# Optimization experiments

Hardware: AMD Instinct MI355X
Metric: run time of the kernel (lower is better)

The kernel has to match this reference:

```python
import jax, jax.numpy as jnp
import numpy as np

N, E, IN_F, H1, F1, H2, F2, OUT_F = 50000, 800000, 128, 4, 32, 1, 64, 2
NEG_SLOPE = 0.2  # PyG GATConv default


def setup_inputs() -> dict:
    key = jax.random.key(0)
    ks = jax.random.split(key, 10)
    p = lambda k, shp: jax.random.normal(k, shp, jnp.float32) * 0.1
    return {
        "x": jax.random.normal(ks[0], (N, IN_F), jnp.float32),
        "edge_index": jax.random.randint(ks[1], (2, E), 0, N),
        "W1": p(ks[2], (IN_F, H1 * F1)),
        "att_s1": p(ks[3], (H1, F1)),
        "att_d1": p(ks[4], (H1, F1)),
        "b1": jnp.zeros((H1 * F1,), jnp.float32),
        "W2": p(ks[5], (H1 * F1, H2 * F2)),
        "att_s2": p(ks[6], (H2, F2)),
        "att_d2": p(ks[7], (H2, F2)),
        "b2": jnp.zeros((F2,), jnp.float32),
        "Wl": p(ks[8], (F2, OUT_F)),
        "bl": jnp.zeros((OUT_F,), jnp.float32),
    }


def _gat_conv(x, src, dst, W, att_s, att_d, bias, concat):
    # PyG GATConv: per-head linear, leaky-relu attention logits,
    # segment-softmax over incoming edges of each dst, scatter-add aggregate.
    n = x.shape[0]
    H, F = att_s.shape
    h = (x @ W).reshape(n, H, F)                        # [N, H, F]
    a_s = jnp.einsum('nhf,hf->nh', h, att_s)            # [N, H]
    a_d = jnp.einsum('nhf,hf->nh', h, att_d)
    logits = jax.nn.leaky_relu(a_s[src] + a_d[dst], NEG_SLOPE)  # [Etot, H]
    m = jax.ops.segment_max(logits, dst, num_segments=n)
    e = jnp.exp(logits - m[dst])
    denom = jax.ops.segment_sum(e, dst, num_segments=n)
    alpha = e / denom[dst]                              # segment softmax
    msg = h[src] * alpha[:, :, None]                    # [Etot, H, F]
    out = jax.ops.segment_sum(msg, dst, num_segments=n)  # [N, H, F]
    out = out.reshape(n, H * F) if concat else out.mean(axis=1)
    return out + bias


def reference(x, edge_index, W1, att_s1, att_d1, b1, W2, att_s2, att_d2, b2, Wl, bl):
    n = x.shape[0]
    loops = jnp.arange(n, dtype=edge_index.dtype)       # add_self_loops=True
    src = jnp.concatenate([edge_index[0], loops])
    dst = jnp.concatenate([edge_index[1], loops])
    h = jax.nn.elu(_gat_conv(x, src, dst, W1, att_s1, att_d1, b1, True))
    h = jax.nn.elu(_gat_conv(h, src, dst, W2, att_s2, att_d2, b2, False))
    pooled = h.sum(axis=0, keepdims=True)               # global_add_pool, batch=0
    out = pooled @ Wl + bl
    return pooled, out
```

## Files before the change

### kernel.cpp

```cpp
#include <hip/hip_runtime.h>

#define N_NODES 50000
#define N_EDGES 800000
#define NB 196
#define P1_BLOCKS 256
#define EPB 3125
#define BH_SIZE (NB * P1_BLOCKS)
#define GEMM_BLOCKS ((N_NODES + 63) / 64)

__device__ __forceinline__ float lrelu(float x) { return fmaxf(x, 0.2f * x); }
__device__ __forceinline__ float elu(float x) { return x > 0.f ? x : __expf(x) - 1.f; }

typedef float f32x2 __attribute__((ext_vector_type(2)));

__device__ __forceinline__ float bfl(unsigned u) { return __uint_as_float(u << 16); }
__device__ __forceinline__ float bfh(unsigned u) { return __uint_as_float(u & 0xffff0000u); }
__device__ __forceinline__ unsigned f2bf_rn(float x) {
  unsigned u = __float_as_uint(x);
  return (u + 0x7fffu + ((u >> 16) & 1u)) >> 16;
}
__device__ __forceinline__ unsigned pack2bf(float a, float b) {
  return f2bf_rn(a) | (f2bf_rn(b) << 16);
}

__device__ __forceinline__ int block_excl_scan(int v, int* total_out) {
  int lane = threadIdx.x & 63;
  int wid = threadIdx.x >> 6;
  int x = v;
#pragma unroll
  for (int off = 1; off < 64; off <<= 1) {
    int u = __shfl_up(x, off);
    if (lane >= off) x += u;
  }
  __shared__ int wsum[4];
  if (lane == 63) wsum[wid] = x;
  __syncthreads();
  int add = 0;
#pragma unroll
  for (int k = 0; k < 4; ++k)
    if (k < wid) add += wsum[k];
  if (total_out) *total_out = wsum[0] + wsum[1] + wsum[2] + wsum[3];
  return x + add - v;
}

__global__ __launch_bounds__(256) void hist1_kernel(const int* __restrict__ ei, int* __restrict__ bh) {
  __shared__ int cnt[NB];
  for (int t = threadIdx.x; t < NB; t += 256) cnt[t] = 0;
  __syncthreads();
  int start = blockIdx.x * EPB;
  for (int i = start + threadIdx.x; i < start + EPB; i += 256)
    atomicAdd(&cnt[ei[N_EDGES + i] >> 8], 1);
  __syncthreads();
  for (int t = threadIdx.x; t < NB; t += 256)
    bh[t * P1_BLOCKS + blockIdx.x] = cnt[t];
}

__global__ __launch_bounds__(256) void scan_part_kernel(const int* __restrict__ bh, int* __restrict__ bhP,
                                                        int* __restrict__ blocksum) {
  int g = blockIdx.x * 256 + threadIdx.x;
  int v = bh[g];
  int total;
  int ex = block_excl_scan(v, &total);
  bhP[g] = ex;
  if (threadIdx.x == 0) blocksum[blockIdx.x] = total;
}

__global__ __launch_bounds__(256) void scan_top_kernel(const int* __restrict__ blocksum, int* __restrict__ blockoff) {
  int t = threadIdx.x;
  int v = (t < NB) ? blocksum[t] : 0;
  int ex = block_excl_scan(v, nullptr);
  if (t < NB) blockoff[t] = ex;
}

__global__ __launch_bounds__(256) void scatter1_kernel(const int* __restrict__ ei, const int* __restrict__ bhP,
                                                       const int* __restrict__ blockoff, int2* __restrict__ eb) {
  __shared__ int cur[NB];
  for (int t = threadIdx.x; t < NB; t += 256) cur[t] = 0;
  __syncthreads();
  int start = blockIdx.x * EPB;
  for (int i = start + threadIdx.x; i < start + EPB; i += 256) {
    int dst = ei[N_EDGES + i];
    int src = ei[i];
    int bin = dst >> 8;
    int r = atomicAdd(&cur[bin], 1);
    int idx = bin * P1_BLOCKS + blockIdx.x;
    int pos = bhP[idx] + blockoff[bin] + r;
    eb[pos] = make_int2(src, dst);
  }
}

__global__ __launch_bounds__(256) void bucket_csr_kernel(const int2* __restrict__ eb, const int* __restrict__ blockoff,
                                                         int* __restrict__ rowptrF, int* __restrict__ col) {
  __shared__ int cnt[256];
  __shared__ int basel[256];
  __shared__ int cur[256];
  int b = blockIdx.x;
  int t = threadIdx.x;
  cnt[t] = 0;
  cur[t] = 0;
  __syncthreads();
  int start = blockoff[b];
  int end = (b == NB - 1) ? N_EDGES : blockoff[b + 1];
  for (int i = start + t; i < end; i += 256)
    atomicAdd(&cnt[eb[i].y & 255], 1);
  __syncthreads();
  int ex = block_excl_scan(cnt[t], nullptr);
  basel[t] = start + ex;
  int g = b * 256 + t;
  if (g < N_NODES) rowptrF[g] = start + ex;
  if (g == N_NODES) rowptrF[N_NODES] = N_EDGES;
  __syncthreads();
  for (int i = start + t; i < end; i += 256) {
    int2 e = eb[i];
    int d8 = e.y & 255;
    int r = atomicAdd(&cur[d8], 1);
    col[basel[d8] + r] = e.x;
  }
}

#define XS_STRIDE 36
template <int COLS, bool ABF16>
__device__ __forceinline__ void gemm_body(int bx, const void* __restrict__ Ap, const float* __restrict__ W,
                                          const float* __restrict__ atts, const float* __restrict__ attd,
                                          unsigned* __restrict__ Yb, float* __restrict__ as_out,
                                          float* __restrict__ ad_out) {
  constexpr int CPT = COLS / 16;
  constexpr int G = COLS / 4;
  __shared__ float ws[32 * COLS];
  __shared__ float xs[64 * XS_STRIDE];
  int t = threadIdx.x;
  int rbase = bx * 64;
  int tx = t & 15, ty = t >> 4;
  float acc[4][CPT];
#pragma unroll
  for (int r = 0; r < 4; ++r)
#pragma unroll
    for (int c = 0; c < CPT; ++c) acc[r][c] = 0.f;

  const float4* W4 = (const float4*)W;
  float4* ws4 = (float4*)ws;
  for (int kt = 0; kt < 4; ++kt) {
    for (int i = t; i < 32 * G; i += 256) {
      int k = i / G;
      int g = i - k * G;
      int c4g = g & (CPT / 4 - 1);
      int txg = g / (CPT / 4);
      ws4[k * G + c4g * 16 + txg] = W4[kt * 32 * G + i];
    }
    if constexpr (ABF16) {
      const uint4* A4 = (const uint4*)Ap;
      {
        int i = t;
        int row = i >> 2, q = i & 3;
        int gr = rbase + row; if (gr >= N_NODES) gr = N_NODES - 1;
        uint4 u = A4[gr * 16 + kt * 4 + q];
        float4 lo = make_float4(bfl(u.x), bfh(u.x), bfl(u.y), bfh(u.y));
        float4 hi = make_float4(bfl(u.z), bfh(u.z), bfl(u.w), bfh(u.w));
        float4* dst = (float4*)&xs[row * XS_STRIDE + q * 8];
        dst[0] = lo; dst[1] = hi;
      }
    } else {
      const float4* A4 = (const float4*)Ap;
      for (int i = t; i < 512; i += 256) {
        int row = i >> 3, kc = i & 7;
        int gr = rbase + row; if (gr >= N_NODES) gr = N_NODES - 1;
        *(float4*)&xs[row * XS_STRIDE + kc * 4] = A4[gr * 32 + kt * 8 + kc];
      }
    }
    __syncthreads();
#pragma unroll 8
    for (int k = 0; k < 32; ++k) {
      float xr[4];
#pragma unroll
      for (int r = 0; r < 4; ++r) xr[r] = xs[(ty * 4 + r) * XS_STRIDE + k];
#pragma unroll
      for (int c4 = 0; c4 < CPT / 4; ++c4) {
        float4 wv = ws4[k * G + c4 * 16 + tx];
#pragma unroll
        for (int r = 0; r < 4; ++r) {
          acc[r][c4 * 4 + 0] += xr[r] * wv.x;
          acc[r][c4 * 4 + 1] += xr[r] * wv.y;
          acc[r][c4 * 4 + 2] += xr[r] * wv.z;
          acc[r][c4 * 4 + 3] += xr[r] * wv.w;
        }
      }
    }
    __syncthreads();
  }

  if constexpr (COLS == 128) {
    int h = tx >> 2;
    int base = h * 32 + (tx & 3) * 8;
#pragma unroll
    for (int r = 0; r < 4; ++r) {
      float ps = 0.f, pd = 0.f;
#pragma unroll
      for (int c = 0; c < 8; ++c) {
        ps += acc[r][c] * atts[base + c];
        pd += acc[r][c] * attd[base + c];
      }
      ps += __shfl_xor(ps, 1); pd += __shfl_xor(pd, 1);
      ps += __shfl_xor(ps, 2); pd += __shfl_xor(pd, 2);
      int row = rbase + ty * 4 + r;
      if ((tx & 3) == 0 && row < N_NODES) {
        as_out[row * 4 + h] = ps;
        ad_out[row * 4 + h] = pd;
      }
    }
  } else {
#pragma unroll
    for (int r = 0; r < 4; ++r) {
      float ps = 0.f, pd = 0.f;
#pragma unroll
      for (int c = 0; c < 4; ++c) {
        ps += acc[r][c] * atts[tx * 4 + c];
        pd += acc[r][c] * attd[tx * 4 + c];
      }
#pragma unroll
      for (int off = 1; off < 16; off <<= 1) {
        ps += __shfl_xor(ps, off);
        pd += __shfl_xor(pd, off);
      }
      int row = rbase + ty * 4 + r;
      if (tx == 0 && row < N_NODES) {
        as_out[row] = ps;
        ad_out[row] = pd;
      }
    }
  }

#pragma unroll
  for (int r = 0; r < 4; ++r) {
    int row = rbase + ty * 4 + r;
    if (row < N_NODES) {
      if constexpr (CPT == 8) {
        unsigned lo = __builtin_amdgcn_cvt_pk_fp8_f32(acc[r][0], acc[r][1], 0, false);
        lo = __builtin_amdgcn_cvt_pk_fp8_f32(acc[r][2], acc[r][3], lo, true);
        unsigned hi = __builtin_amdgcn_cvt_pk_fp8_f32(acc[r][4], acc[r][5], 0, false);
        hi = __builtin_amdgcn_cvt_pk_fp8_f32(acc[r][6], acc[r][7], hi, true);
        ((uint2*)Yb)[row * 16 + tx] = make_uint2(lo, hi);
      } else {
        unsigned u = __builtin_amdgcn_cvt_pk_fp8_f32(acc[r][0], acc[r][1], 0, false);
        u = __builtin_amdgcn_cvt_pk_fp8_f32(acc[r][2], acc[r][3], u, true);
        Yb[row * 16 + tx] = u;
      }
    }
  }
}

__global__ __launch_bounds__(256) void gemm128_kernel(const float* __restrict__ x, const float* __restrict__ W1,
                                                      const float* __restrict__ atts, const float* __restrict__ attd,
                                                      unsigned* __restrict__ h1b, float* __restrict__ as1,
                                                      float* __restrict__ ad1) {
  gemm_body<128, false>(blockIdx.x, x, W1, atts, attd, h1b, as1, ad1);
}

__global__ __launch_bounds__(256) void gemm64_kernel(const unsigned* __restrict__ h1eb, const float* __restrict__ W2,
                                                     const float* __restrict__ atts, const float* __restrict__ attd,
                                                     unsigned* __restrict__ h2b, float* __restrict__ as2,
                                                     float* __restrict__ ad2) {
  gemm_body<64, true>(blockIdx.x, h1eb, W2, atts, attd, h2b, as2, ad2);
}

__global__ __launch_bounds__(256) void agg1_kernel(const uint2* __restrict__ h1f8, const int* __restrict__ rowptr,
                                                   const int* __restrict__ col, const float* __restrict__ as1,
                                                   const float* __restrict__ ad1, const float4* __restrict__ b1v,
                                                   uint4* __restrict__ h1eb4) {
  int n = (blockIdx.x * 256 + threadIdx.x) >> 6;
  int lane = threadIdx.x & 63;
  int slot = lane >> 4;
  int fo = lane & 15;
  int h = fo >> 2;
  int beg = rowptr[n], end = rowptr[n + 1];
  float adh = ad1[n * 4 + h];

  f32x2 acc2[4];
#pragma unroll
  for (int j = 0; j < 4; ++j) acc2[j] = (f32x2){0.f, 0.f};
  float esum = 0.f;

#define ACC_EDGE1(E)                                               \
  {                                                                \
    int src = col[E];                                              \
    float a = __expf(lrelu(as1[src * 4 + h] + adh));               \
    esum += a;                                                     \
    f32x2 av = {a, a};                                             \
    uint2 uu = h1f8[src * 16 + fo];                                \
    f32x2 p0 = __builtin_amdgcn_cvt_pk_f32_fp8(uu.x, false);       \
    f32x2 p1 = __builtin_amdgcn_cvt_pk_f32_fp8(uu.x, true);        \
    f32x2 p2 = __builtin_amdgcn_cvt_pk_f32_fp8(uu.y, false);       \
    f32x2 p3 = __builtin_amdgcn_cvt_pk_f32_fp8(uu.y, true);        \
    acc2[0] += av * p0; acc2[1] += av * p1;                        \
    acc2[2] += av * p2; acc2[3] += av * p3;                        \
  }

  int i = beg;
  for (; i + 16 <= end; i += 16) {
#pragma unroll
    for (int u = 0; u < 4; ++u) ACC_EDGE1(i + u * 4 + slot);
  }
  for (; i + 4 <= end; i += 4) ACC_EDGE1(i + slot);
  int rem = end - i;
  if (slot < rem) ACC_EDGE1(i + slot);
#undef ACC_EDGE1
  if (slot == 0) {
    float a = __expf(lrelu(as1[n * 4 + h] + adh));
    esum += a;
    f32x2 av = {a, a};
    uint2 uu = h1f8[n * 16 + fo];
    f32x2 p0 = __builtin_amdgcn_cvt_pk_f32_fp8(uu.x, false);
    f32x2 p1 = __builtin_amdgcn_cvt_pk_f32_fp8(uu.x, true);
    f32x2 p2 = __builtin_amdgcn_cvt_pk_f32_fp8(uu.y, false);
    f32x2 p3 = __builtin_amdgcn_cvt_pk_f32_fp8(uu.y, true);
    acc2[0] += av * p0; acc2[1] += av * p1;
    acc2[2] += av * p2; acc2[3] += av * p3;
  }
#pragma unroll
  for (int j = 0; j < 4; ++j) {
    acc2[j].x += __shfl_xor(acc2[j].x, 16);
    acc2[j].y += __shfl_xor(acc2[j].y, 16);
    acc2[j].x += __shfl_xor(acc2[j].x, 32);
    acc2[j].y += __shfl_xor(acc2[j].y, 32);
  }
  esum += __shfl_xor(esum, 16);
  esum += __shfl_xor(esum, 32);
  if (slot == 0) {
    float dsc = 1.f / esum;
    float4 b0 = b1v[fo * 2], b1 = b1v[fo * 2 + 1];
    float f0 = elu(acc2[0].x * dsc + b0.x), f1 = elu(acc2[0].y * dsc + b0.y);
    float f2 = elu(acc2[1].x * dsc + b0.z), f3 = elu(acc2[1].y * dsc + b0.w);
    float f4 = elu(acc2[2].x * dsc + b1.x), f5 = elu(acc2[2].y * dsc + b1.y);
    float f6 = elu(acc2[3].x * dsc + b1.z), f7 = elu(acc2[3].y * dsc + b1.w);
    uint4 o;
    o.x = pack2bf(f0, f1); o.y = pack2bf(f2, f3);
    o.z = pack2bf(f4, f5); o.w = pack2bf(f6, f7);
    h1eb4[n * 16 + fo] = o;
  }
}

__global__ __launch_bounds__(256) void agg2_kernel(const uint2* __restrict__ h2f8, const int* __restrict__ rowptr,
                                                   const int* __restrict__ col, const float* __restrict__ as2,
                                                   const float* __restrict__ ad2, const float4* __restrict__ b2v,
                                                   float* __restrict__ pooled) {
  __shared__ float red[4][64];
  int n = (blockIdx.x * 256 + threadIdx.x) >> 6;
  int lane = threadIdx.x & 63;
  int wid = threadIdx.x >> 6;
  int slot = lane >> 3;
  int fo = lane & 7;
  int beg = rowptr[n], end = rowptr[n + 1];
  float ad = ad2[n];

  f32x2 acc2[4];
#pragma unroll
  for (int j = 0; j < 4; ++j) acc2[j] = (f32x2){0.f, 0.f};
  float esum = 0.f;

#define ACC_EDGE2(E)                                               \
  {                                                                \
    int src = col[E];                                              \
    float a = __expf(lrelu(as2[src] + ad));                        \
    esum += a;                                                     \
    f32x2 av = {a, a};                                             \
    uint2 uu = h2f8[src * 8 + fo];                                 \
    f32x2 p0 = __builtin_amdgcn_cvt_pk_f32_fp8(uu.x, false);       \
    f32x2 p1 = __builtin_amdgcn_cvt_pk_f32_fp8(uu.x, true);        \
    f32x2 p2 = __builtin_amdgcn_cvt_pk_f32_fp8(uu.y, false);       \
    f32x2 p3 = __builtin_amdgcn_cvt_pk_f32_fp8(uu.y, true);        \
    acc2[0] += av * p0; acc2[1] += av * p1;                        \
    acc2[2] += av * p2; acc2[3] += av * p3;                        \
  }

  int i = beg;
  for (; i + 32 <= end; i += 32) {
#pragma unroll
    for (int u = 0; u < 4; ++u) ACC_EDGE2(i + u * 8 + slot);
  }
  for (; i + 8 <= end; i += 8) ACC_EDGE2(i + slot);
  int rem = end - i;
  if (slot < rem) ACC_EDGE2(i + slot);
#undef ACC_EDGE2
  if (slot == 0) {
    float a = __expf(lrelu(as2[n] + ad));
    esum += a;
    f32x2 av = {a, a};
    uint2 uu = h2f8[n * 8 + fo];
    f32x2 p0 = __builtin_amdgcn_cvt_pk_f32_fp8(uu.x, false);
    f32x2 p1 = __builtin_amdgcn_cvt_pk_f32_fp8(uu.x, true);
    f32x2 p2 = __builtin_amdgcn_cvt_pk_f32_fp8(uu.y, false);
    f32x2 p3 = __builtin_amdgcn_cvt_pk_f32_fp8(uu.y, true);
    acc2[0] += av * p0; acc2[1] += av * p1;
    acc2[2] += av * p2; acc2[3] += av * p3;
  }
#pragma unroll
  for (int j = 0; j < 4; ++j) {
#pragma unroll
    for (int off = 8; off <= 32; off <<= 1) {
      acc2[j].x += __shfl_xor(acc2[j].x, off);
      acc2[j].y += __shfl_xor(acc2[j].y, off);
    }
  }
  esum += __shfl_xor(esum, 8);
  esum += __shfl_xor(esum, 16);
  esum += __shfl_xor(esum, 32);
  if (slot == 0) {
    float dsc = 1.f / esum;
    float4 b0 = b2v[fo * 2], b1 = b2v[fo * 2 + 1];
    red[wid][fo * 8 + 0] = elu(acc2[0].x * dsc + b0.x);
    red[wid][fo * 8 + 1] = elu(acc2[0].y * dsc + b0.y);
    red[wid][fo * 8 + 2] = elu(acc2[1].x * dsc + b0.z);
    red[wid][fo * 8 + 3] = elu(acc2[1].y * dsc + b0.w);
    red[wid][fo * 8 + 4] = elu(acc2[2].x * dsc + b1.x);
    red[wid][fo * 8 + 5] = elu(acc2[2].y * dsc + b1.y);
    red[wid][fo * 8 + 6] = elu(acc2[3].x * dsc + b1.z);
    red[wid][fo * 8 + 7] = elu(acc2[3].y * dsc + b1.w);
  }
  __syncthreads();
  if (threadIdx.x < 64) {
    float sum = red[0][threadIdx.x] + red[1][threadIdx.x] + red[2][threadIdx.x] + red[3][threadIdx.x];
    atomicAdd(&pooled[(blockIdx.x & 63) * 64 + threadIdx.x], sum);
  }
}

__global__ void final_kernel(const float* __restrict__ pooledS, const float* __restrict__ Wl,
                             const float* __restrict__ bl, float* __restrict__ out) {
  __shared__ float p[64];
  int t = threadIdx.x;
  float v = 0.f;
  for (int k = 0; k < 64; ++k) v += pooledS[k * 64 + t];
  p[t] = v;
  out[t] = v;
  __syncthreads();
  if (t < 2) {
    float s = bl[t];
    for (int k = 0; k < 64; ++k) s += p[k] * Wl[k * 2 + t];
    out[64 + t] = s;
  }
}

extern "C" void kernel_launch(void* const* d_in, const int* in_sizes, int n_in,
                              void* d_out, int out_size, void* d_ws, size_t ws_size,
                              hipStream_t stream) {
  (void)in_sizes; (void)n_in; (void)out_size; (void)ws_size;
  const float* x     = (const float*)d_in[0];
  const int*   ei    = (const int*)d_in[1];
  const float* W1    = (const float*)d_in[2];
  const float* atts1 = (const float*)d_in[3];
  const float* attd1 = (const float*)d_in[4];
  const float* b1    = (const float*)d_in[5];
  const float* W2    = (const float*)d_in[6];
  const float* atts2 = (const float*)d_in[7];
  const float* attd2 = (const float*)d_in[8];
  const float* b2    = (const float*)d_in[9];
  const float* Wl    = (const float*)d_in[10];
  const float* bl    = (const float*)d_in[11];
  float* out = (float*)d_out;

  char* w = (char*)d_ws;
  unsigned* h1b  = (unsigned*)w; w += (size_t)N_NODES * 128;
  unsigned* h1eb = (unsigned*)w; w += (size_t)N_NODES * 128 * 2;
  unsigned* h2b  = (unsigned*)w; w += (size_t)N_NODES * 64;
  float* as1  = (float*)w; w += (size_t)N_NODES * 16;
  float* ad1  = (float*)w; w += (size_t)N_NODES * 16;
  float* as2  = (float*)w; w += (size_t)N_NODES * 4;
  float* ad2  = (float*)w; w += (size_t)N_NODES * 4;
  float* pooled = (float*)w; w += 64 * 64 * 4;
  int* rowptrF = (int*)w; w += (size_t)(N_NODES + 1) * 4 + 12;
  int* col    = (int*)w; w += (size_t)N_EDGES * 4;
  int2* eb    = (int2*)w; w += (size_t)N_EDGES * 8;
  int* bh     = (int*)w; w += (size_t)BH_SIZE * 4;
  int* bhP    = (int*)w; w += (size_t)BH_SIZE * 4;
  int* blocksum = (int*)w; w += 256 * 4;
  int* blockoff = (int*)w; w += 256 * 4;

  (void)hipMemsetAsync(pooled, 0, 64 * 64 * 4, stream);

  hist1_kernel<<<P1_BLOCKS, 256, 0, stream>>>(ei, bh);
  scan_part_kernel<<<BH_SIZE / 256, 256, 0, stream>>>(bh, bhP, blocksum);
  scan_top_kernel<<<1, 256, 0, stream>>>(blocksum, blockoff);
  scatter1_kernel<<<P1_BLOCKS, 256, 0, stream>>>(ei, bhP, blockoff, eb);
  bucket_csr_kernel<<<NB, 256, 0, stream>>>(eb, blockoff, rowptrF, col);

  gemm128_kernel<<<GEMM_BLOCKS, 256, 0, stream>>>(x, W1, atts1, attd1, h1b, as1, ad1);
  agg1_kernel<<<N_NODES / 4, 256, 0, stream>>>((const uint2*)h1b, rowptrF, col, as1, ad1,
                                               (const float4*)b1, (uint4*)h1eb);

  gemm64_kernel<<<GEMM_BLOCKS, 256, 0, stream>>>(h1eb, W2, atts2, attd2, h2b, as2, ad2);
  agg2_kernel<<<N_NODES / 4, 256, 0, stream>>>((const uint2*)h2b, rowptrF, col, as2, ad2,
                                               (const float4*)b2, pooled);

  final_kernel<<<1, 64, 0, stream>>>(pooled, Wl, bl, out);
}
```

Before: 230.8 us.

## Fuse scatter with layer-1 GEMM and fold final reduction into agg2

After: 452.0 us. +95.9%, slower.

```diff
diff --git a/kernel.cpp b/kernel.cpp
--- a/kernel.cpp
+++ b/kernel.cpp
@@ -70,52 +70,6 @@
   int v = (t < NB) ? blocksum[t] : 0;
   int ex = block_excl_scan(v, nullptr);
   if (t < NB) blockoff[t] = ex;
-}
-
-__global__ __launch_bounds__(256) void scatter1_kernel(const int* __restrict__ ei, const int* __restrict__ bhP,
-                                                       const int* __restrict__ blockoff, int2* __restrict__ eb) {
-  __shared__ int cur[NB];
-  for (int t = threadIdx.x; t < NB; t += 256) cur[t] = 0;
-  __syncthreads();
-  int start = blockIdx.x * EPB;
-  for (int i = start + threadIdx.x; i < start + EPB; i += 256) {
-    int dst = ei[N_EDGES + i];
-    int src = ei[i];
-    int bin = dst >> 8;
-    int r = atomicAdd(&cur[bin], 1);
-    int idx = bin * P1_BLOCKS + blockIdx.x;
-    int pos = bhP[idx] + blockoff[bin] + r;
-    eb[pos] = make_int2(src, dst);
-  }
-}
-
-__global__ __launch_bounds__(256) void bucket_csr_kernel(const int2* __restrict__ eb, const int* __restrict__ blockoff,
-                                                         int* __restrict__ rowptrF, int* __restrict__ col) {
-  __shared__ int cnt[256];
-  __shared__ int basel[256];
-  __shared__ int cur[256];
-  int b = blockIdx.x;
-  int t = threadIdx.x;
-  cnt[t] = 0;
-  cur[t] = 0;
-  __syncthreads();
-  int start = blockoff[b];
-  int end = (b == NB - 1) ? N_EDGES : blockoff[b + 1];
-  for (int i = start + t; i < end; i += 256)
-    atomicAdd(&cnt[eb[i].y & 255], 1);
-  __syncthreads();
-  int ex = block_excl_scan(cnt[t], nullptr);
-  basel[t] = start + ex;
-  int g = b * 256 + t;
-  if (g < N_NODES) rowptrF[g] = start + ex;
-  if (g == N_NODES) rowptrF[N_NODES] = N_EDGES;
-  __syncthreads();
-  for (int i = start + t; i < end; i += 256) {
-    int2 e = eb[i];
-    int d8 = e.y & 255;
-    int r = atomicAdd(&cur[d8], 1);
-    col[basel[d8] + r] = e.x;
-  }
 }
 
 #define XS_STRIDE 36
@@ -248,11 +202,56 @@
   }
 }
 
-__global__ __launch_bounds__(256) void gemm128_kernel(const float* __restrict__ x, const float* __restrict__ W1,
-                                                      const float* __restrict__ atts, const float* __restrict__ attd,
-                                                      unsigned* __restrict__ h1b, float* __restrict__ as1,
-                                                      float* __restrict__ ad1) {
-  gemm_body<128, false>(blockIdx.x, x, W1, atts, attd, h1b, as1, ad1);
+__global__ __launch_bounds__(256) void scatter1_gemm128_kernel(
+    const int* __restrict__ ei, const int* __restrict__ bhP, const int* __restrict__ blockoff,
+    int2* __restrict__ eb, const float* __restrict__ x, const float* __restrict__ W1,
+    const float* __restrict__ atts1, const float* __restrict__ attd1, unsigned* __restrict__ h1b,
+    float* __restrict__ as1, float* __restrict__ ad1) {
+  if (blockIdx.x < P1_BLOCKS) {
+    __shared__ int cur[NB];
+    for (int t = threadIdx.x; t < NB; t += 256) cur[t] = 0;
+    __syncthreads();
+    int start = blockIdx.x * EPB;
+    for (int i = start + threadIdx.x; i < start + EPB; i += 256) {
+      int dst = ei[N_EDGES + i];
+      int src = ei[i];
+      int bin = dst >> 8;
+      int r = atomicAdd(&cur[bin], 1);
+      int pos = bhP[bin * P1_BLOCKS + blockIdx.x] + blockoff[bin] + r;
+      eb[pos] = make_int2(src, dst);
+    }
+    return;
+  }
+  gemm_body<128, false>(blockIdx.x - P1_BLOCKS, x, W1, atts1, attd1, h1b, as1, ad1);
+}
+
+__global__ __launch_bounds__(256) void bucket_csr_kernel(const int2* __restrict__ eb, const int* __restrict__ blockoff,
+                                                         int* __restrict__ rowptrF, int* __restrict__ col) {
+  __shared__ int cnt[256];
+  __shared__ int basel[256];
+  __shared__ int cur[256];
+  int b = blockIdx.x;
+  int t = threadIdx.x;
+  cnt[t] = 0;
+  cur[t] = 0;
+  __syncthreads();
+  int start = blockoff[b];
+  int end = (b == NB - 1) ? N_EDGES : blockoff[b + 1];
+  for (int i = start + t; i < end; i += 256)
+    atomicAdd(&cnt[eb[i].y & 255], 1);
+  __syncthreads();
+  int ex = block_excl_scan(cnt[t], nullptr);
+  basel[t] = start + ex;
+  int g = b * 256 + t;
+  if (g < N_NODES) rowptrF[g] = start + ex;
+  if (g == N_NODES) rowptrF[N_NODES] = N_EDGES;
+  __syncthreads();
+  for (int i = start + t; i < end; i += 256) {
+    int2 e = eb[i];
+    int d8 = e.y & 255;
+    int r = atomicAdd(&cur[d8], 1);
+    col[basel[d8] + r] = e.x;
+  }
 }
 
 __global__ __launch_bounds__(256) void gemm64_kernel(const unsigned* __restrict__ h1eb, const float* __restrict__ W2,
@@ -341,7 +340,9 @@
 __global__ __launch_bounds__(256) void agg2_kernel(const uint2* __restrict__ h2f8, const int* __restrict__ rowptr,
                                                    const int* __restrict__ col, const float* __restrict__ as2,
                                                    const float* __restrict__ ad2, const float4* __restrict__ b2v,
-                                                   float* __restrict__ pooled) {
+                                                   float* __restrict__ pooled, int* __restrict__ done,
+                                                   const float* __restrict__ Wl, const float* __restrict__ bl,
+                                                   float* __restrict__ out) {
   __shared__ float red[4][64];
   int n = (blockIdx.x * 256 + threadIdx.x) >> 6;
   int lane = threadIdx.x & 63;
@@ -420,16 +421,23 @@
     float sum = red[0][threadIdx.x] + red[1][threadIdx.x] + red[2][threadIdx.x] + red[3][threadIdx.x];
     atomicAdd(&pooled[(blockIdx.x & 63) * 64 + threadIdx.x], sum);
   }
-}
-
-__global__ void final_kernel(const float* __restrict__ pooledS, const float* __restrict__ Wl,
-                             const float* __restrict__ bl, float* __restrict__ out) {
-  __shared__ float p[64];
+  __syncthreads();
+  __shared__ int lastflag;
+  if (threadIdx.x == 0) {
+    __threadfence();
+    lastflag = (atomicAdd(done, 1) == (int)gridDim.x - 1);
+  }
+  __syncthreads();
+  if (!lastflag) return;
+  __threadfence();
   int t = threadIdx.x;
-  float v = 0.f;
-  for (int k = 0; k < 64; ++k) v += pooledS[k * 64 + t];
-  p[t] = v;
-  out[t] = v;
+  float* p = &red[0][0];
+  if (t < 64) {
+    float v = 0.f;
+    for (int k = 0; k < 64; ++k) v += atomicAdd(&pooled[k * 64 + t], 0.f);
+    p[t] = v;
+    out[t] = v;
+  }
   __syncthreads();
   if (t < 2) {
     float s = bl[t];
@@ -465,6 +473,7 @@
   float* as2  = (float*)w; w += (size_t)N_NODES * 4;
   float* ad2  = (float*)w; w += (size_t)N_NODES * 4;
   float* pooled = (float*)w; w += 64 * 64 * 4;
+  int* done   = (int*)w; w += 16;
   int* rowptrF = (int*)w; w += (size_t)(N_NODES + 1) * 4 + 12;
   int* col    = (int*)w; w += (size_t)N_EDGES * 4;
   int2* eb    = (int2*)w; w += (size_t)N_EDGES * 8;
@@ -473,21 +482,19 @@
   int* blocksum = (int*)w; w += 256 * 4;
   int* blockoff = (int*)w; w += 256 * 4;
 
-  (void)hipMemsetAsync(pooled, 0, 64 * 64 * 4, stream);
+  (void)hipMemsetAsync(pooled, 0, 64 * 64 * 4 + 16, stream);
 
   hist1_kernel<<<P1_BLOCKS, 256, 0, stream>>>(ei, bh);
   scan_part_kernel<<<BH_SIZE / 256, 256, 0, stream>>>(bh, bhP, blocksum);
   scan_top_kernel<<<1, 256, 0, stream>>>(blocksum, blockoff);
-  scatter1_kernel<<<P1_BLOCKS, 256, 0, stream>>>(ei, bhP, blockoff, eb);
+  scatter1_gemm128_kernel<<<P1_BLOCKS + GEMM_BLOCKS, 256, 0, stream>>>(ei, bhP, blockoff, eb,
+                                                                       x, W1, atts1, attd1, h1b, as1, ad1);
   bucket_csr_kernel<<<NB, 256, 0, stream>>>(eb, blockoff, rowptrF, col);
 
-  gemm128_kernel<<<GEMM_BLOCKS, 256, 0, stream>>>(x, W1, atts1, attd1, h1b, as1, ad1);
   agg1_kernel<<<N_NODES / 4, 256, 0, stream>>>((const uint2*)h1b, rowptrF, col, as1, ad1,
                                                (const float4*)b1, (uint4*)h1eb);
 
   gemm64_kernel<<<GEMM_BLOCKS, 256, 0, stream>>>(h1eb, W2, atts2, attd2, h2b, as2, ad2);
   agg2_kernel<<<N_NODES / 4, 256, 0, stream>>>((const uint2*)h2b, rowptrF, col, as2, ad2,
-                                               (const float4*)b2, pooled);
-
-  final_kernel<<<1, 64, 0, stream>>>(pooled, Wl, bl, out);
-}
+                                               (const float4*)b2, pooled, done, Wl, bl, out);
+}
```
